# Optimization experiments

Hardware: AMD Instinct MI355X
Metric: run time of the kernel (lower is better)

Reference implementation:

```python
import jax, jax.numpy as jnp
import numpy as np

NUM_LEAVES = 256
EPS = 1e-6
SHARPNESS = 1.0   # init_sharpness, non-trainable buffer
BIAS_SHIFT = -2.0


def _generalized_gcd(w1, w2, lambd):
    # lambd: per-node bias -> andness via sigmoid; broadcast over batch
    lam = jax.nn.sigmoid(lambd)
    a = jnp.abs(w1) + EPS
    b = jnp.abs(w2) + EPS
    return lam * jnp.minimum(a, b) + (1.0 - lam) * jnp.maximum(a, b)


def setup_inputs() -> dict:
    key = jax.random.key(0)
    ks = jax.random.split(key, 6)
    B, L = 65536, NUM_LEAVES
    x = jax.random.normal(ks[0], (B, L), jnp.float32)
    # xavier-like scale for the leaf projection
    W_leaf = jax.random.normal(ks[1], (L, L), jnp.float32) * (1.0 / np.sqrt(L))
    weights = jax.random.uniform(ks[2], (L - 1, 2), jnp.float32, 0.5, 1.5)
    biases = jax.random.uniform(ks[3], (L - 1,), jnp.float32) * 0.1
    w_out = jax.random.normal(ks[4], (1, 1), jnp.float32)
    b_out = jnp.full((1,), 0.5, jnp.float32)
    return {"x": x, "W_leaf": W_leaf, "weights": weights,
            "biases": biases, "w_out": w_out, "b_out": b_out}


def reference(x, W_leaf, weights, biases, w_out, b_out):
    # InputToLeafFC: sigmoid(sharpness * (x @ W^T + bias_shift))
    leaf = jax.nn.sigmoid(SHARPNESS * (x @ W_leaf.T + BIAS_SHIFT))  # (B, L)

    # The original pops two nodes from the front of the queue and appends the
    # result; for a power-of-two leaf count this is exactly a level-by-level
    # pairwise tree reduction, with node weights consumed in order.
    cur = leaf
    off = 0
    n = cur.shape[1]
    while n > 1:  # log2(L) levels, each fully vectorized over (batch, pairs)
        m = n // 2
        w = weights[off:off + m]   # (m, 2)
        b = biases[off:off + m]    # (m,)
        left = cur[:, 0::2] * w[:, 0]
        right = cur[:, 1::2] * w[:, 1]
        cur = _generalized_gcd(left, right, b)  # (B, m)
        off += m
        n = m
    # fc_out: Linear(1,1) then sigmoid -> (B, 1)
    return jax.nn.sigmoid(cur * w_out[0, 0] + b_out[0])
```

## Files before the change

kernel.cpp:

```cpp
#include <hip/hip_runtime.h>
#include <stdint.h>


#define EPS 1e-6f
#define LOG2E 1.44269504088896340736f
#define WSTR 264

typedef __attribute__((ext_vector_type(8))) short short8;
typedef __attribute__((ext_vector_type(4))) short short4_t;
typedef __attribute__((ext_vector_type(4))) float float4_t;

__device__ __forceinline__ float fast_sigmoid(float z) {
    float e = __builtin_amdgcn_exp2f(-z * LOG2E);
    return __builtin_amdgcn_rcpf(1.0f + e);
}

__device__ __forceinline__ short f2bf(float f) {
    uint32_t u = __builtin_bit_cast(uint32_t, f);
    u += 0x7FFFu + ((u >> 16) & 1u);
    return (short)(u >> 16);
}

__device__ __forceinline__ float ggcd(float l, float r, float lam) {
    float a = fabsf(l) + EPS;
    float b = fabsf(r) + EPS;
    float mn = fminf(a, b);
    float mx = fmaxf(a, b);
    return fmaf(lam, mn - mx, mx);
}

__global__ __launch_bounds__(256)
void convert_w_kernel(const float* __restrict__ Wl, short* __restrict__ img) {
    int t = blockIdx.x * 256 + threadIdx.x;
    int j   = t >> 6;
    int kc4 = t & 63;
    const float4* Wv4 = (const float4*)Wl;
    float4 w4 = Wv4[j * 64 + kc4];
    int p = ((j & 15) << 4) | (j >> 4);
    short4_t s4;
    s4.x = f2bf(w4.x); s4.y = f2bf(w4.y); s4.z = f2bf(w4.z); s4.w = f2bf(w4.w);
    *(short4_t*)&img[p * WSTR + kc4 * 4] = s4;
}

__global__ __launch_bounds__(1024, 4)
void btln_main(const float* __restrict__ x, const short* __restrict__ img,
               const float* __restrict__ wts, const float* __restrict__ bia,
               const float* __restrict__ wout, const float* __restrict__ bout,
               float* __restrict__ out) {
    __shared__ short Ws[256 * WSTR];
    __shared__ float w0v[256], w1v[256], lamv[256];

    const int tid  = threadIdx.x;
    const int lane = tid & 63;
    const int wv   = tid >> 6;
    const int c0   = lane & 15;
    const int q    = lane >> 4;

    {
        const uint4* img4 = (const uint4*)img;
        uint4* ws4 = (uint4*)Ws;
        #pragma unroll
        for (int it = 0; it < 9; ++it) {
            int i = it * 1024 + tid;
            if (i < (256 * WSTR * 2) / 16) ws4[i] = img4[i];
        }
    }
    if (tid < 255) {
        w0v[tid]  = wts[2 * tid];
        w1v[tid]  = wts[2 * tid + 1];
        lamv[tid] = fast_sigmoid(bia[tid]);
    }
    __syncthreads();

    const int group   = blockIdx.x * 16 + wv;
    const int rowbase = group * 16;
    const float* xrow = x + (size_t)(rowbase + c0) * 256;

    float4_t acc[16];
    #pragma unroll
    for (int t = 0; t < 16; ++t) acc[t] = (float4_t){0.f, 0.f, 0.f, 0.f};

    #pragma unroll
    for (int kk = 0; kk < 256; kk += 32) {
        const float4* ap = (const float4*)(xrow + kk + q * 8);
        float4 a0 = ap[0], a1 = ap[1];
        short8 af;
        af[0] = f2bf(a0.x); af[1] = f2bf(a0.y); af[2] = f2bf(a0.z); af[3] = f2bf(a0.w);
        af[4] = f2bf(a1.x); af[5] = f2bf(a1.y); af[6] = f2bf(a1.z); af[7] = f2bf(a1.w);
        #pragma unroll
        for (int t = 0; t < 16; ++t) {
            short8 bf = *(const short8*)&Ws[(t * 16 + c0) * WSTR + kk + q * 8];
            acc[t] = __builtin_amdgcn_mfma_f32_16x16x32_bf16(af, bf, acc[t], 0, 0, 0);
        }
    }

    const float wo = wout[0];
    const float bo = bout[0];

    float res[4];
    #pragma unroll
    for (int r = 0; r < 4; ++r) {
        float s[16];
        #pragma unroll
        for (int t = 0; t < 16; ++t) s[t] = fast_sigmoid(acc[t][r] - 2.0f);
        #pragma unroll
        for (int tp = 0; tp < 8; ++tp) {
            int n = c0 * 8 + tp;
            s[tp] = ggcd(s[2*tp] * w0v[n], s[2*tp+1] * w1v[n], lamv[n]);
        }
        #pragma unroll
        for (int tp = 0; tp < 4; ++tp) {
            int n = 128 + c0 * 4 + tp;
            s[tp] = ggcd(s[2*tp] * w0v[n], s[2*tp+1] * w1v[n], lamv[n]);
        }
        #pragma unroll
        for (int tp = 0; tp < 2; ++tp) {
            int n = 192 + c0 * 2 + tp;
            s[tp] = ggcd(s[2*tp] * w0v[n], s[2*tp+1] * w1v[n], lamv[n]);
        }
        {
            int n = 224 + c0;
            res[r] = ggcd(s[0] * w0v[n], s[1] * w1v[n], lamv[n]);
        }
    }

    const int offs[4] = {240, 248, 252, 254};
    #pragma unroll
    for (int k = 0; k < 4; ++k) {
        int n = offs[k] + (c0 >> (k + 1));
        float w0n = w0v[n], w1n = w1v[n], lm = lamv[n];
        bool isLeft = ((c0 >> k) & 1) == 0;
        #pragma unroll
        for (int r = 0; r < 4; ++r) {
            float other = __shfl_xor(res[r], 1 << k, 64);
            float lf = isLeft ? res[r] : other;
            float rt = isLeft ? other  : res[r];
            res[r] = ggcd(lf * w0n, rt * w1n, lm);
        }
    }

    if (c0 == 0) {
        #pragma unroll
        for (int r = 0; r < 4; ++r) {
            out[rowbase + q * 4 + r] = fast_sigmoid(fmaf(res[r], wo, bo));
        }
    }
}

extern "C" void kernel_launch(void* const* d_in, const int* in_sizes, int n_in,
                              void* d_out, int out_size, void* d_ws, size_t ws_size,
                              hipStream_t stream) {
    const float* x   = (const float*)d_in[0];
    const float* Wl  = (const float*)d_in[1];
    const float* wts = (const float*)d_in[2];
    const float* bia = (const float*)d_in[3];
    const float* wo  = (const float*)d_in[4];
    const float* bo  = (const float*)d_in[5];
    float* out = (float*)d_out;
    short* img = (short*)d_ws;

    convert_w_kernel<<<dim3(64), dim3(256), 0, stream>>>(Wl, img);

    const int rows = out_size;
    dim3 grid(rows / (16 * 16)), block(1024);
    btln_main<<<grid, block, 0, stream>>>(x, img, wts, bia, wo, bo, out);
}
```

Baseline: 116.0 us.

## Pack tree params as float4, software-pipeline x loads, restructure tree epilogue

The per-node tree weights and sigmoid(bias) are now packed by the prep kernel into one float4 array in the workspace, and the main kernel loads it with a single LDS array read per node instead of three scalar reads. The K loop is no longer unrolled and prefetches the next x tile into registers while the current tile is converted and fed to MFMA. The tree reduction now works level by level across all four rows, so each parameter load is shared by four rows. Rolling the loop may reduce instruction-level overlap, and the prefetch keeps extra registers live.

Result: no change. 115.4 us (-0.6%).

```diff
diff --git a/kernel.cpp b/kernel.cpp
--- a/kernel.cpp
+++ b/kernel.cpp
@@ -5,6 +5,8 @@
 #define EPS 1e-6f
 #define LOG2E 1.44269504088896340736f
 #define WSTR 264
+#define WIMG_SHORTS (256 * WSTR)
+#define PARAM_OFF_B (WIMG_SHORTS * 2)
 
 typedef __attribute__((ext_vector_type(8))) short short8;
 typedef __attribute__((ext_vector_type(4))) short short4_t;
@@ -30,7 +32,9 @@
 }
 
 __global__ __launch_bounds__(256)
-void convert_w_kernel(const float* __restrict__ Wl, short* __restrict__ img) {
+void convert_w_kernel(const float* __restrict__ Wl,
+                      const float* __restrict__ wts, const float* __restrict__ bia,
+                      short* __restrict__ img) {
     int t = blockIdx.x * 256 + threadIdx.x;
     int j   = t >> 6;
     int kc4 = t & 63;
@@ -40,15 +44,24 @@
     short4_t s4;
     s4.x = f2bf(w4.x); s4.y = f2bf(w4.y); s4.z = f2bf(w4.z); s4.w = f2bf(w4.w);
     *(short4_t*)&img[p * WSTR + kc4 * 4] = s4;
+
+    if (blockIdx.x == 0) {
+        float4* pv = (float4*)((char*)img + PARAM_OFF_B);
+        if (threadIdx.x < 255) {
+            int n = threadIdx.x;
+            pv[n] = make_float4(wts[2 * n], wts[2 * n + 1], fast_sigmoid(bia[n]), 0.f);
+        } else if (threadIdx.x == 255) {
+            pv[255] = make_float4(0.f, 0.f, 0.f, 0.f);
+        }
+    }
 }
 
 __global__ __launch_bounds__(1024, 4)
 void btln_main(const float* __restrict__ x, const short* __restrict__ img,
-               const float* __restrict__ wts, const float* __restrict__ bia,
                const float* __restrict__ wout, const float* __restrict__ bout,
                float* __restrict__ out) {
-    __shared__ short Ws[256 * WSTR];
-    __shared__ float w0v[256], w1v[256], lamv[256];
+    __shared__ short Ws[WIMG_SHORTS];
+    __shared__ float4 pv[256];
 
     const int tid  = threadIdx.x;
     const int lane = tid & 63;
@@ -59,91 +72,102 @@
     {
         const uint4* img4 = (const uint4*)img;
         uint4* ws4 = (uint4*)Ws;
+        const int n16 = (WIMG_SHORTS * 2) / 16;
         #pragma unroll
         for (int it = 0; it < 9; ++it) {
             int i = it * 1024 + tid;
-            if (i < (256 * WSTR * 2) / 16) ws4[i] = img4[i];
+            if (i < n16) ws4[i] = img4[i];
         }
-    }
-    if (tid < 255) {
-        w0v[tid]  = wts[2 * tid];
-        w1v[tid]  = wts[2 * tid + 1];
-        lamv[tid] = fast_sigmoid(bia[tid]);
+        if (tid < 256) {
+            const float4* gpv = (const float4*)((const char*)img + PARAM_OFF_B);
+            pv[tid] = gpv[tid];
+        }
     }
     __syncthreads();
 
     const int group   = blockIdx.x * 16 + wv;
     const int rowbase = group * 16;
-    const float* xrow = x + (size_t)(rowbase + c0) * 256;
+    const float4* xv  = (const float4*)(x + (size_t)(rowbase + c0) * 256);
 
     float4_t acc[16];
     #pragma unroll
     for (int t = 0; t < 16; ++t) acc[t] = (float4_t){0.f, 0.f, 0.f, 0.f};
 
-    #pragma unroll
-    for (int kk = 0; kk < 256; kk += 32) {
-        const float4* ap = (const float4*)(xrow + kk + q * 8);
-        float4 a0 = ap[0], a1 = ap[1];
+    float4 a0 = xv[q * 2];
+    float4 a1 = xv[q * 2 + 1];
+    #pragma unroll 1
+    for (int kt = 0; kt < 8; ++kt) {
+        const int ktn = (kt < 7) ? kt + 1 : 7;
+        float4 b0 = xv[ktn * 8 + q * 2];
+        float4 b1 = xv[ktn * 8 + q * 2 + 1];
+
         short8 af;
         af[0] = f2bf(a0.x); af[1] = f2bf(a0.y); af[2] = f2bf(a0.z); af[3] = f2bf(a0.w);
         af[4] = f2bf(a1.x); af[5] = f2bf(a1.y); af[6] = f2bf(a1.z); af[7] = f2bf(a1.w);
+
+        const int kk = kt * 32;
         #pragma unroll
         for (int t = 0; t < 16; ++t) {
             short8 bf = *(const short8*)&Ws[(t * 16 + c0) * WSTR + kk + q * 8];
             acc[t] = __builtin_amdgcn_mfma_f32_16x16x32_bf16(af, bf, acc[t], 0, 0, 0);
         }
+        a0 = b0; a1 = b1;
     }
 
-    const float wo = wout[0];
-    const float bo = bout[0];
-
+    #pragma unroll
+    for (int t = 0; t < 16; ++t) {
+        #pragma unroll
+        for (int r = 0; r < 4; ++r) acc[t][r] = fast_sigmoid(acc[t][r] - 2.0f);
+    }
+    #pragma unroll
+    for (int tp = 0; tp < 8; ++tp) {
+        float4 p = pv[c0 * 8 + tp];
+        #pragma unroll
+        for (int r = 0; r < 4; ++r)
+            acc[tp][r] = ggcd(acc[2*tp][r] * p.x, acc[2*tp+1][r] * p.y, p.z);
+    }
+    #pragma unroll
+    for (int tp = 0; tp < 4; ++tp) {
+        float4 p = pv[128 + c0 * 4 + tp];
+        #pragma unroll
+        for (int r = 0; r < 4; ++r)
+            acc[tp][r] = ggcd(acc[2*tp][r] * p.x, acc[2*tp+1][r] * p.y, p.z);
+    }
+    #pragma unroll
+    for (int tp = 0; tp < 2; ++tp) {
+        float4 p = pv[192 + c0 * 2 + tp];
+        #pragma unroll
+        for (int r = 0; r < 4; ++r)
+            acc[tp][r] = ggcd(acc[2*tp][r] * p.x, acc[2*tp+1][r] * p.y, p.z);
+    }
     float res[4];
-    #pragma unroll
-    for (int r = 0; r < 4; ++r) {
-        float s[16];
+    {
+        float4 p = pv[224 + c0];
         #pragma unroll
-        for (int t = 0; t < 16; ++t) s[t] = fast_sigmoid(acc[t][r] - 2.0f);
-        #pragma unroll
-        for (int tp = 0; tp < 8; ++tp) {
-            int n = c0 * 8 + tp;
-            s[tp] = ggcd(s[2*tp] * w0v[n], s[2*tp+1] * w1v[n], lamv[n]);
-        }
-        #pragma unroll
-        for (int tp = 0; tp < 4; ++tp) {
-            int n = 128 + c0 * 4 + tp;
-            s[tp] = ggcd(s[2*tp] * w0v[n], s[2*tp+1] * w1v[n], lamv[n]);
-        }
-        #pragma unroll
-        for (int tp = 0; tp < 2; ++tp) {
-            int n = 192 + c0 * 2 + tp;
-            s[tp] = ggcd(s[2*tp] * w0v[n], s[2*tp+1] * w1v[n], lamv[n]);
-        }
-        {
-            int n = 224 + c0;
-            res[r] = ggcd(s[0] * w0v[n], s[1] * w1v[n], lamv[n]);
-        }
+        for (int r = 0; r < 4; ++r)
+            res[r] = ggcd(acc[0][r] * p.x, acc[1][r] * p.y, p.z);
     }
 
     const int offs[4] = {240, 248, 252, 254};
     #pragma unroll
     for (int k = 0; k < 4; ++k) {
-        int n = offs[k] + (c0 >> (k + 1));
-        float w0n = w0v[n], w1n = w1v[n], lm = lamv[n];
+        float4 p = pv[offs[k] + (c0 >> (k + 1))];
         bool isLeft = ((c0 >> k) & 1) == 0;
         #pragma unroll
         for (int r = 0; r < 4; ++r) {
             float other = __shfl_xor(res[r], 1 << k, 64);
             float lf = isLeft ? res[r] : other;
             float rt = isLeft ? other  : res[r];
-            res[r] = ggcd(lf * w0n, rt * w1n, lm);
+            res[r] = ggcd(lf * p.x, rt * p.y, p.z);
         }
     }
 
     if (c0 == 0) {
+        const float wo = wout[0];
+        const float bo = bout[0];
         #pragma unroll
-        for (int r = 0; r < 4; ++r) {
+        for (int r = 0; r < 4; ++r)
             out[rowbase + q * 4 + r] = fast_sigmoid(fmaf(res[r], wo, bo));
-        }
     }
 }
 
@@ -159,9 +183,9 @@
     float* out = (float*)d_out;
     short* img = (short*)d_ws;
 
-    convert_w_kernel<<<dim3(64), dim3(256), 0, stream>>>(Wl, img);
+    convert_w_kernel<<<dim3(64), dim3(256), 0, stream>>>(Wl, wts, bia, img);
 
     const int rows = out_size;
-    dim3 grid(rows / (16 * 16)), block(1024);
-    btln_main<<<grid, block, 0, stream>>>(x, img, wts, bia, wo, bo, out);
+    dim3 grid(rows / 256), block(1024);
+    btln_main<<<grid, block, 0, stream>>>(x, img, wo, bo, out);
 }
```
